# Optimization experiments

Hardware: AMD Instinct MI355X
Metric: run time of the kernel (lower is better)

Reference implementation:

```python
import jax, jax.numpy as jnp
import numpy as np

H = 16            # L-BFGS history length
N = 4_000_000     # number of parameters
HIGH = jax.lax.Precision.HIGHEST


def setup_inputs() -> dict:
    key = jax.random.key(0)
    k1, k2, k3 = jax.random.split(key, 3)
    # Small-scale steps so inner products are well conditioned.
    y = jax.random.normal(k1, (H, N), jnp.float32) * 0.01           # S_k: parameter diffs
    g = y + 0.1 * jax.random.normal(k2, (H, N), jnp.float32) * 0.01  # Y_k: grad diffs, s_i.g_i > 0
    pytree = jax.random.normal(k3, (N,), jnp.float32)
    sy = jnp.dot(y, g.T, precision=HIGH)                 # [H,H] s_i . y_j
    cross = jnp.tril(sy, k=-1)                           # L_k (strictly lower triangular)
    diag = jnp.diag(sy)                                  # diag(D_k), positive by construction
    s_inner = jnp.dot(y, y.T, precision=HIGH)            # S^T S
    return {
        "pytree": pytree,
        "y_diff_history": y,
        "grad_diff_history": g,
        "y_diff_grad_diff_cross_inner": cross,
        "y_diff_grad_diff_inner": diag,
        "y_diff_cross_inner": s_inner,
        "index_start": 21,  # > H: buffer full, circular-roll branch active
    }


def reference(pytree, y_diff_history, grad_diff_history,
              y_diff_grad_diff_cross_inner, y_diff_grad_diff_inner,
              y_diff_cross_inner, index_start):
    h = y_diff_history.shape[0]
    idx = (index_start - 1) % h
    s_last = y_diff_history[idx]
    g_last = grad_diff_history[idx]
    curvature = jnp.dot(s_last, g_last, precision=HIGH)
    gamma = jnp.where(curvature > 0,
                      jnp.dot(g_last, g_last, precision=HIGH) / curvature,
                      jnp.float32(1.0))
    d = jnp.where(y_diff_grad_diff_inner == 0, 1.0, y_diff_grad_diff_inner)
    L = y_diff_grad_diff_cross_inner
    # J J^T = gamma * S^T S + L D^-1 L^T
    J_square = gamma * y_diff_cross_inner + jnp.dot(L / d, L.T, precision=HIGH)
    J = jnp.linalg.cholesky(J_square)
    # Project input onto the two history bases: [2H]
    top = jnp.einsum('hn,n->h', grad_diff_history, pytree, precision=HIGH)
    bot = gamma * jnp.einsum('hn,n->h', y_diff_history, pytree, precision=HIGH)
    descent = jnp.concatenate([top, bot])
    roll_by = -(index_start % h)

    def maybe_roll(v, r):
        return jax.lax.cond(index_start <= h, lambda x: x, lambda x: jnp.roll(x, r), v)

    descent = descent.at[:h].set(maybe_roll(descent[:h], roll_by))
    descent = descent.at[h:].set(maybe_roll(descent[h:], roll_by))
    sqrt_d = jnp.sqrt(d)
    low_tri = jnp.block([
        [jnp.diag(sqrt_d), jnp.zeros((h, h), descent.dtype)],
        [-L / sqrt_d, J],
    ])
    descent = jax.scipy.linalg.solve_triangular(low_tri, descent, lower=True)
    upper_tri = low_tri.T
    upper_tri = upper_tri.at[:h].set(-upper_tri[:h])
    descent = jax.scipy.linalg.solve_triangular(upper_tri, descent, lower=False)
    descent = descent.at[:h].set(maybe_roll(descent[:h], -roll_by))
    descent = descent.at[h:].set(maybe_roll(descent[h:], -roll_by))
    out = (gamma * pytree
           - jnp.einsum('h,hn->n', descent[:h], grad_diff_history, precision=HIGH)
           - gamma * jnp.einsum('h,hn->n', descent[h:], y_diff_history, precision=HIGH))
    return out
```

## Files before the change

kernel.cpp:

```cpp
#include <hip/hip_runtime.h>

#define HH 16
#define RED_VALS 34

__global__ __launch_bounds__(256) void lbfgs_reduce(
    const float* __restrict__ p, const float* __restrict__ y,
    const float* __restrict__ g, const int* __restrict__ idxp,
    float* __restrict__ partials, int n) {
  const int is = idxp[0];
  const int hidx = ((is - 1) % HH + HH) % HH;
  float acc[RED_VALS];
#pragma unroll
  for (int j = 0; j < RED_VALS; ++j) acc[j] = 0.f;

  const int tid = blockIdx.x * blockDim.x + threadIdx.x;
  const int nth = gridDim.x * blockDim.x;
  const int nchunk = n >> 2;
  const float4* __restrict__ p4 = reinterpret_cast<const float4*>(p);

  for (int c = tid; c < nchunk; c += nth) {
    float4 pv = p4[c];
#pragma unroll
    for (int i = 0; i < HH; ++i) {
      const float4 gv = reinterpret_cast<const float4*>(g + (size_t)i * n)[c];
      const float4 yv = reinterpret_cast<const float4*>(y + (size_t)i * n)[c];
      acc[i]      += gv.x * pv.x + gv.y * pv.y + gv.z * pv.z + gv.w * pv.w;
      acc[HH + i] += yv.x * pv.x + yv.y * pv.y + yv.z * pv.z + yv.w * pv.w;
      if (i == hidx) {
        acc[32] += yv.x * gv.x + yv.y * gv.y + yv.z * gv.z + yv.w * gv.w;
        acc[33] += gv.x * gv.x + gv.y * gv.y + gv.z * gv.z + gv.w * gv.w;
      }
    }
  }
  for (int c = (nchunk << 2) + tid; c < n; c += nth) {
    float pv = p[c];
#pragma unroll
    for (int i = 0; i < HH; ++i) {
      float gv = g[(size_t)i * n + c];
      float yv = y[(size_t)i * n + c];
      acc[i] += gv * pv;
      acc[HH + i] += yv * pv;
      if (i == hidx) { acc[32] += yv * gv; acc[33] += gv * gv; }
    }
  }
#pragma unroll
  for (int j = 0; j < RED_VALS; ++j) {
    float v = acc[j];
#pragma unroll
    for (int off = 32; off > 0; off >>= 1) v += __shfl_down(v, off);
    acc[j] = v;
  }
  __shared__ float red[4][RED_VALS];
  const int wave = threadIdx.x >> 6, lane = threadIdx.x & 63;
  if (lane == 0) {
#pragma unroll
    for (int j = 0; j < RED_VALS; ++j) red[wave][j] = acc[j];
  }
  __syncthreads();
  if (threadIdx.x < RED_VALS) {
    float s = red[0][threadIdx.x] + red[1][threadIdx.x] +
              red[2][threadIdx.x] + red[3][threadIdx.x];
    partials[(size_t)blockIdx.x * RED_VALS + threadIdx.x] = s;
  }
}

__global__ __launch_bounds__(256) void lbfgs_solve(
    const float* __restrict__ partials, int nblk,
    const float* __restrict__ Lmat, const float* __restrict__ diag,
    const float* __restrict__ sinner, const int* __restrict__ idxp,
    float* __restrict__ coeff) {
  __shared__ float sums[RED_VALS];
  __shared__ float wred[RED_VALS][4];
  const int wave = threadIdx.x >> 6, lane = threadIdx.x & 63;
  for (int j = 0; j < RED_VALS; ++j) {
    float v = 0.f;
    for (int b = threadIdx.x; b < nblk; b += 256)
      v += partials[(size_t)b * RED_VALS + j];
#pragma unroll
    for (int off = 32; off > 0; off >>= 1) v += __shfl_down(v, off);
    if (lane == 0) wred[j][wave] = v;
  }
  __syncthreads();
  if (threadIdx.x < RED_VALS)
    sums[threadIdx.x] = wred[threadIdx.x][0] + wred[threadIdx.x][1] +
                        wred[threadIdx.x][2] + wred[threadIdx.x][3];
  __syncthreads();

  __shared__ float Lsh[HH][HH];
  __shared__ float dd[HH], sqd[HH];
  __shared__ float Jsq[HH][HH];
  __shared__ float gamma_s;
  __shared__ float x[2 * HH];
  {
    int i = threadIdx.x >> 4, j = threadIdx.x & 15;
    if (threadIdx.x < 256) Lsh[i][j] = Lmat[i * HH + j];
  }
  if (threadIdx.x < HH) {
    float dv = diag[threadIdx.x];
    float ddv = (dv == 0.f) ? 1.f : dv;
    dd[threadIdx.x] = ddv;
    sqd[threadIdx.x] = sqrtf(ddv);
  }
  if (threadIdx.x == 0) {
    float cur = sums[32], gg = sums[33];
    gamma_s = (cur > 0.f) ? (gg / cur) : 1.f;
  }
  __syncthreads();
  {
    int i = threadIdx.x >> 4, j = threadIdx.x & 15;
    float v = gamma_s * sinner[i * HH + j];
#pragma unroll
    for (int k = 0; k < HH; ++k) v += Lsh[i][k] * Lsh[j][k] / dd[k];
    Jsq[i][j] = v;
  }
  __syncthreads();
  if (threadIdx.x == 0) {
    for (int c = 0; c < HH; ++c) {
      float s = Jsq[c][c];
      for (int k = 0; k < c; ++k) s -= Jsq[c][k] * Jsq[c][k];
      float dv = sqrtf(s);
      Jsq[c][c] = dv;
      float inv = 1.f / dv;
      for (int r = c + 1; r < HH; ++r) {
        float s2 = Jsq[r][c];
        for (int k = 0; k < c; ++k) s2 -= Jsq[r][k] * Jsq[c][k];
        Jsq[r][c] = s2 * inv;
      }
    }
    const int is = idxp[0];
    const int sh = (is <= HH) ? 0 : (is % HH);
    const float gamma = gamma_s;
    for (int k = 0; k < HH; ++k) {
      x[k]      = sums[(k + sh) & (HH - 1)];
      x[HH + k] = gamma * sums[HH + ((k + sh) & (HH - 1))];
    }
    for (int i = 0; i < HH; ++i) x[i] /= sqd[i];
    for (int i = 0; i < HH; ++i) {
      float s = x[HH + i];
      for (int j = 0; j < HH; ++j) s += (Lsh[i][j] / sqd[j]) * x[j];
      for (int j = 0; j < i; ++j) s -= Jsq[i][j] * x[HH + j];
      x[HH + i] = s / Jsq[i][i];
    }
    for (int i = HH - 1; i >= 0; --i) {
      float s = x[HH + i];
      for (int j = i + 1; j < HH; ++j) s -= Jsq[j][i] * x[HH + j];
      x[HH + i] = s / Jsq[i][i];
    }
    for (int i = 0; i < HH; ++i) {
      float s = x[i];
      for (int j = 0; j < HH; ++j) s -= (Lsh[j][i] / sqd[i]) * x[HH + j];
      x[i] = s / (-sqd[i]);
    }
    coeff[0] = gamma;
    for (int k = 0; k < HH; ++k) {
      coeff[1 + k]      = x[(k - sh + HH) & (HH - 1)];
      coeff[1 + HH + k] = gamma * x[HH + ((k - sh + HH) & (HH - 1))];
    }
  }
}

__global__ __launch_bounds__(256) void lbfgs_output(
    const float* __restrict__ p, const float* __restrict__ y,
    const float* __restrict__ g, const float* __restrict__ coeff,
    float* __restrict__ out, int n) {
  const float gamma = coeff[0];
  float a[HH], b[HH];
#pragma unroll
  for (int i = 0; i < HH; ++i) {
    a[i] = coeff[1 + i];
    b[i] = coeff[1 + HH + i];
  }
  const int tid = blockIdx.x * blockDim.x + threadIdx.x;
  const int nth = gridDim.x * blockDim.x;
  const int nchunk = n >> 2;
  const float4* __restrict__ p4 = reinterpret_cast<const float4*>(p);
  float4* __restrict__ out4 = reinterpret_cast<float4*>(out);
  for (int c = tid; c < nchunk; c += nth) {
    float4 pv = p4[c];
    float ox = gamma * pv.x, oy = gamma * pv.y;
    float oz = gamma * pv.z, ow = gamma * pv.w;
#pragma unroll
    for (int i = 0; i < HH; ++i) {
      const float4 gv = reinterpret_cast<const float4*>(g + (size_t)i * n)[c];
      const float4 yv = reinterpret_cast<const float4*>(y + (size_t)i * n)[c];
      ox -= a[i] * gv.x + b[i] * yv.x;
      oy -= a[i] * gv.y + b[i] * yv.y;
      oz -= a[i] * gv.z + b[i] * yv.z;
      ow -= a[i] * gv.w + b[i] * yv.w;
    }
    out4[c] = make_float4(ox, oy, oz, ow);
  }
  for (int c = (nchunk << 2) + tid; c < n; c += nth) {
    float pv = p[c];
    float o = gamma * pv;
#pragma unroll
    for (int i = 0; i < HH; ++i)
      o -= a[i] * g[(size_t)i * n + c] + b[i] * y[(size_t)i * n + c];
    out[c] = o;
  }
}

extern "C" void kernel_launch(void* const* d_in, const int* in_sizes, int n_in,
                              void* d_out, int out_size, void* d_ws, size_t ws_size,
                              hipStream_t stream) {
  const float* p      = (const float*)d_in[0];
  const float* y      = (const float*)d_in[1];
  const float* g      = (const float*)d_in[2];
  const float* Lmat   = (const float*)d_in[3];
  const float* diag   = (const float*)d_in[4];
  const float* sinner = (const float*)d_in[5];
  const int*   idxp   = (const int*)d_in[6];
  float* out = (float*)d_out;
  float* wsf = (float*)d_ws;
  const int n = in_sizes[0];

  int nblk = 1024;
  size_t need = (size_t)(nblk * RED_VALS + 64) * sizeof(float);
  if (ws_size < need) {
    long avail = (long)(ws_size / sizeof(float)) - 64;
    nblk = (int)(avail / RED_VALS);
    if (nblk < 1) nblk = 1;
    if (nblk > 1024) nblk = 1024;
  }
  float* partials = wsf;
  float* coeff = wsf + (size_t)nblk * RED_VALS;

  lbfgs_reduce<<<dim3(nblk), dim3(256), 0, stream>>>(p, y, g, idxp, partials, n);
  lbfgs_solve<<<dim3(1), dim3(256), 0, stream>>>(partials, nblk, Lmat, diag,
                                                 sinner, idxp, coeff);
  lbfgs_output<<<dim3(nblk), dim3(256), 0, stream>>>(p, y, g, coeff, out, n);
}
```

Before: 258.4 us.

## Use one-chunk-per-thread reduction grid with batched loads and transposed partials

Adds a reduction kernel that launches one thread per float4 chunk (about 3900 blocks). Each thread issues all 32 history-row loads up front, behind a scheduling barrier, to raise memory-level parallelism. Partials are stored transposed so the solve kernel reads them coalesced, and the output kernel's grid grows to 2048 blocks. The cost is a much larger partials array (34 x ~3900 floats) that the single-block solve kernel must sum, and high register pressure from 32 float4 values held per thread.

```diff
diff --git a/kernel.cpp b/kernel.cpp
--- a/kernel.cpp
+++ b/kernel.cpp
@@ -2,11 +2,93 @@
 
 #define HH 16
 #define RED_VALS 34
-
-__global__ __launch_bounds__(256) void lbfgs_reduce(
+#define OUTBLK 2048
+
+__global__ __launch_bounds__(256) void lbfgs_reduce_line(
     const float* __restrict__ p, const float* __restrict__ y,
     const float* __restrict__ g, const int* __restrict__ idxp,
-    float* __restrict__ partials, int n) {
+    float* __restrict__ partials, int nblk, int n) {
+  const int c = blockIdx.x * 256 + threadIdx.x;
+  const int nchunk = n >> 2;
+  const int is = idxp[0];
+  const int hidx = ((is - 1) % HH + HH) % HH;
+
+  float accg[HH], accy[HH];
+#pragma unroll
+  for (int i = 0; i < HH; ++i) { accg[i] = 0.f; accy[i] = 0.f; }
+  float ac = 0.f, agg = 0.f;
+
+  if (c < nchunk) {
+    const float4 pv = reinterpret_cast<const float4*>(p)[c];
+    float4 gv[HH], yv[HH];
+#pragma unroll
+    for (int i = 0; i < HH; ++i)
+      gv[i] = reinterpret_cast<const float4*>(g + (size_t)i * n)[c];
+#pragma unroll
+    for (int i = 0; i < HH; ++i)
+      yv[i] = reinterpret_cast<const float4*>(y + (size_t)i * n)[c];
+    __builtin_amdgcn_sched_barrier(0);
+#pragma unroll
+    for (int i = 0; i < HH; ++i) {
+      accg[i] = gv[i].x * pv.x + gv[i].y * pv.y + gv[i].z * pv.z + gv[i].w * pv.w;
+      accy[i] = yv[i].x * pv.x + yv[i].y * pv.y + yv[i].z * pv.z + yv[i].w * pv.w;
+      float dyg = yv[i].x * gv[i].x + yv[i].y * gv[i].y +
+                  yv[i].z * gv[i].z + yv[i].w * gv[i].w;
+      float dgg = gv[i].x * gv[i].x + gv[i].y * gv[i].y +
+                  gv[i].z * gv[i].z + gv[i].w * gv[i].w;
+      ac  += (i == hidx) ? dyg : 0.f;
+      agg += (i == hidx) ? dgg : 0.f;
+    }
+  }
+  if (blockIdx.x == 0) {
+    for (int e = (nchunk << 2) + threadIdx.x; e < n; e += 256) {
+      float pv = p[e];
+#pragma unroll
+      for (int i = 0; i < HH; ++i) {
+        float gs = g[(size_t)i * n + e], ys = y[(size_t)i * n + e];
+        accg[i] += gs * pv;
+        accy[i] += ys * pv;
+        ac  += (i == hidx) ? ys * gs : 0.f;
+        agg += (i == hidx) ? gs * gs : 0.f;
+      }
+    }
+  }
+
+  __shared__ float red[4][RED_VALS];
+  const int wave = threadIdx.x >> 6, lane = threadIdx.x & 63;
+#pragma unroll
+  for (int i = 0; i < HH; ++i) {
+    float v = accg[i];
+#pragma unroll
+    for (int off = 32; off > 0; off >>= 1) v += __shfl_down(v, off);
+    if (lane == 0) red[wave][i] = v;
+    float w = accy[i];
+#pragma unroll
+    for (int off = 32; off > 0; off >>= 1) w += __shfl_down(w, off);
+    if (lane == 0) red[wave][HH + i] = w;
+  }
+  {
+    float v = ac;
+#pragma unroll
+    for (int off = 32; off > 0; off >>= 1) v += __shfl_down(v, off);
+    if (lane == 0) red[wave][32] = v;
+    float w = agg;
+#pragma unroll
+    for (int off = 32; off > 0; off >>= 1) w += __shfl_down(w, off);
+    if (lane == 0) red[wave][33] = w;
+  }
+  __syncthreads();
+  if (threadIdx.x < RED_VALS) {
+    float s = red[0][threadIdx.x] + red[1][threadIdx.x] +
+              red[2][threadIdx.x] + red[3][threadIdx.x];
+    partials[(size_t)threadIdx.x * nblk + blockIdx.x] = s;
+  }
+}
+
+__global__ __launch_bounds__(256) void lbfgs_reduce_loop(
+    const float* __restrict__ p, const float* __restrict__ y,
+    const float* __restrict__ g, const int* __restrict__ idxp,
+    float* __restrict__ partials, int nblk, int n) {
   const int is = idxp[0];
   const int hidx = ((is - 1) % HH + HH) % HH;
   float acc[RED_VALS];
@@ -60,12 +142,12 @@
   if (threadIdx.x < RED_VALS) {
     float s = red[0][threadIdx.x] + red[1][threadIdx.x] +
               red[2][threadIdx.x] + red[3][threadIdx.x];
-    partials[(size_t)blockIdx.x * RED_VALS + threadIdx.x] = s;
+    partials[(size_t)threadIdx.x * nblk + blockIdx.x] = s;
   }
 }
 
 __global__ __launch_bounds__(256) void lbfgs_solve(
-    const float* __restrict__ partials, int nblk,
+    const float* __restrict__ partials, int nblkp,
     const float* __restrict__ Lmat, const float* __restrict__ diag,
     const float* __restrict__ sinner, const int* __restrict__ idxp,
     float* __restrict__ coeff) {
@@ -74,8 +156,8 @@
   const int wave = threadIdx.x >> 6, lane = threadIdx.x & 63;
   for (int j = 0; j < RED_VALS; ++j) {
     float v = 0.f;
-    for (int b = threadIdx.x; b < nblk; b += 256)
-      v += partials[(size_t)b * RED_VALS + j];
+    for (int b = threadIdx.x; b < nblkp; b += 256)
+      v += partials[(size_t)j * nblkp + b];
 #pragma unroll
     for (int off = 32; off > 0; off >>= 1) v += __shfl_down(v, off);
     if (lane == 0) wred[j][wave] = v;
@@ -214,19 +296,29 @@
   float* wsf = (float*)d_ws;
   const int n = in_sizes[0];
 
-  int nblk = 1024;
-  size_t need = (size_t)(nblk * RED_VALS + 64) * sizeof(float);
-  if (ws_size < need) {
+  const int nchunk = n >> 2;
+  const int nblk_line = (nchunk + 255) / 256;
+  const size_t need_line = ((size_t)RED_VALS * nblk_line + 64) * sizeof(float);
+
+  if (ws_size >= need_line) {
+    float* partials = wsf;
+    float* coeff = wsf + (size_t)RED_VALS * nblk_line;
+    lbfgs_reduce_line<<<dim3(nblk_line), dim3(256), 0, stream>>>(
+        p, y, g, idxp, partials, nblk_line, n);
+    lbfgs_solve<<<dim3(1), dim3(256), 0, stream>>>(partials, nblk_line, Lmat,
+                                                   diag, sinner, idxp, coeff);
+    lbfgs_output<<<dim3(OUTBLK), dim3(256), 0, stream>>>(p, y, g, coeff, out, n);
+  } else {
+    int nblk = 1024;
     long avail = (long)(ws_size / sizeof(float)) - 64;
-    nblk = (int)(avail / RED_VALS);
-    if (nblk < 1) nblk = 1;
-    if (nblk > 1024) nblk = 1024;
-  }
-  float* partials = wsf;
-  float* coeff = wsf + (size_t)nblk * RED_VALS;
-
-  lbfgs_reduce<<<dim3(nblk), dim3(256), 0, stream>>>(p, y, g, idxp, partials, n);
-  lbfgs_solve<<<dim3(1), dim3(256), 0, stream>>>(partials, nblk, Lmat, diag,
-                                                 sinner, idxp, coeff);
-  lbfgs_output<<<dim3(nblk), dim3(256), 0, stream>>>(p, y, g, coeff, out, n);
-}
+    long cap = avail / RED_VALS;
+    if (cap < nblk) nblk = (int)(cap < 1 ? 1 : cap);
+    float* partials = wsf;
+    float* coeff = wsf + (size_t)RED_VALS * nblk;
+    lbfgs_reduce_loop<<<dim3(nblk), dim3(256), 0, stream>>>(
+        p, y, g, idxp, partials, nblk, n);
+    lbfgs_solve<<<dim3(1), dim3(256), 0, stream>>>(partials, nblk, Lmat,
+                                                   diag, sinner, idxp, coeff);
+    lbfgs_output<<<dim3(OUTBLK), dim3(256), 0, stream>>>(p, y, g, coeff, out, n);
+  }
+}
```

Measured after the change: 425.1 us. 64.5% more time.
